# Kernel tuning notes

Measured on AMD Instinct MI355X. Metric: run time of the kernel, lower is better.

## Reference

```python
import jax, jax.numpy as jnp
import numpy as np

L, B, D = 128, 4096, 300


def setup_inputs() -> dict:
    key = jax.random.key(0)
    k1, k2, k3 = jax.random.split(key, 3)
    sentence = jax.random.normal(k1, (L, B, D), dtype=jnp.float32)
    size = jax.random.randint(k2, (B,), 0, L)  # per-example valid lengths
    # nn.Bilinear(D, D, 1, bias=False) weight, squeezed to [D, D]
    W = jax.random.normal(k3, (D, D), dtype=jnp.float32) * (1.0 / np.sqrt(D))
    return {"sentence": sentence, "size": size, "W": W}


def reference(sentence, size, W):
    # sentence: [L, B, D] seq-first; size: [B] lengths; W: [D, D] bilinear weight
    Ls, Bs, Ds = sentence.shape
    dim = jnp.asarray(Ds, sentence.dtype)
    neg_inf = jnp.asarray(-jnp.inf, sentence.dtype)

    def bil(x, y):
        # elementwise bilinear score x^T W y -> [l, b]
        return jnp.einsum('lbd,de,lbe->lb', x, W, y)

    # symmetrized neighbor score for pairs (l, l-1), l = 1..L-1 -> [L-1, B]
    sym = 0.5 * (bil(sentence[1:], sentence[:-1]) + bil(sentence[:-1], sentence[1:]))

    pad = jnp.full((1, Bs), neg_inf, dtype=sentence.dtype)
    w0 = jnp.concatenate([pad, sym], axis=0)   # prev-neighbor channel; l=0 has no prev
    w2 = jnp.concatenate([sym, pad], axis=0)   # next-neighbor channel; l=L-1 has no next
    w1 = bil(sentence, sentence)               # self channel, always valid

    # padding masks from 'size': channel 0 valid for l < size, channel 2 for l < size-1
    pos = jnp.arange(Ls)[:, None]              # [L, 1]
    w0 = jnp.where(pos < size[None, :], w0, neg_inf)
    w2 = jnp.where(pos < jnp.clip(size - 1, 0)[None, :], w2, neg_inf)

    logits = jnp.stack([w0, w1, w2], axis=-1) / dim   # [L, B, 3]
    w = jax.nn.softmax(logits, axis=-1)               # self channel always finite -> safe

    zero_row = jnp.zeros((1, Bs, Ds), sentence.dtype)
    s_prev = jnp.concatenate([zero_row, sentence[:-1]], axis=0)
    s_next = jnp.concatenate([sentence[1:], zero_row], axis=0)

    # masked channels have exactly zero weight, so padded shifts contribute nothing
    out = w[..., 1:2] * sentence + w[..., 0:1] * s_prev + w[..., 2:3] * s_next
    # dropout(p=0.05) is identity in eval mode
    return out
```

## Files before the change

kernel.cpp:

```cpp
#include <hip/hip_runtime.h>
#include <stdint.h>

#define LL 128
#define BB 4096
#define DD 300
#define DP 320
#define SROW 328

typedef __attribute__((ext_vector_type(8))) short short8;
typedef __attribute__((ext_vector_type(4))) float f32x4;

static constexpr int S16_ELEMS = 129 * SROW;
static constexpr int SMEM_BYTES = S16_ELEMS * 2 + 128 * 5 * 4;

__device__ __forceinline__ unsigned short f2bf(float f) {
    unsigned int u = __builtin_bit_cast(unsigned int, f);
    u = (u + 0x7fffu + ((u >> 16) & 1u)) >> 16;
    return (unsigned short)u;
}
__device__ __forceinline__ float bf2f(unsigned short h) {
    unsigned int u = ((unsigned int)h) << 16;
    return __builtin_bit_cast(float, u);
}

__global__ void prep_w_kernel(const float* __restrict__ W, unsigned short* __restrict__ Wb) {
    int i = blockIdx.x * 256 + threadIdx.x;
    if (i >= DP * DP) return;
    int r = i / DP, c = i % DP;
    float v = 0.0f;
    if (r < DD && c < DD) v = 0.5f * (W[r * DD + c] + W[c * DD + r]);
    Wb[i] = f2bf(v);
}

__global__ __launch_bounds__(512) void fused_kernel(
        const float* __restrict__ sent, const int* __restrict__ sizes,
        const unsigned short* __restrict__ Wb, float* __restrict__ out) {
    extern __shared__ char smem[];
    unsigned short* S16 = (unsigned short*)smem;
    float* q1s = (float*)(smem + S16_ELEMS * 2);
    float* q2s = q1s + 128;
    float* w0s = q2s + 128;
    float* w1s = w0s + 128;
    float* w2s = w1s + 128;

    const int b = blockIdx.x;
    const int t = threadIdx.x;

    for (int idx = t; idx < 128 * 75; idx += 512) {
        int row = idx / 75, c4 = idx % 75;
        const float4 v = ((const float4*)(sent + ((size_t)row * BB + b) * DD))[c4];
        ushort4 h;
        h.x = f2bf(v.x); h.y = f2bf(v.y); h.z = f2bf(v.z); h.w = f2bf(v.w);
        *(ushort4*)&S16[row * SROW + c4 * 4] = h;
    }
    for (int r = t; r < 129; r += 512) {
        #pragma unroll
        for (int c = 300; c < SROW; c += 4) {
            ushort4 z; z.x = 0; z.y = 0; z.z = 0; z.w = 0;
            *(ushort4*)&S16[r * SROW + c] = z;
        }
    }
    for (int c4 = t; c4 < 75; c4 += 512) {
        ushort4 z; z.x = 0; z.y = 0; z.z = 0; z.w = 0;
        *(ushort4*)&S16[128 * SROW + c4 * 4] = z;
    }
    if (t < 256) q1s[t] = 0.0f;
    __syncthreads();

    const int lane = t & 63;
    const int wave = t >> 6;
    const int mw = wave & 3;
    const int nw2 = wave >> 2;
    const int lo = lane & 15;
    const int quad = lane >> 4;

    f32x4 acc[5][4];
    #pragma unroll
    for (int i = 0; i < 5; i++)
        #pragma unroll
        for (int j = 0; j < 4; j++)
            acc[i][j] = (f32x4){0.f, 0.f, 0.f, 0.f};

    #pragma unroll
    for (int kc = 0; kc < 10; kc++) {
        short8 Af[5], Bf[4];
        #pragma unroll
        for (int i = 0; i < 5; i++)
            Af[i] = *(const short8*)&Wb[(16 * (5 * mw + i) + lo) * DP + kc * 32 + quad * 8];
        #pragma unroll
        for (int j = 0; j < 4; j++)
            Bf[j] = *(const short8*)&S16[(16 * (4 * nw2 + j) + lo) * SROW + kc * 32 + quad * 8];
        #pragma unroll
        for (int i = 0; i < 5; i++)
            #pragma unroll
            for (int j = 0; j < 4; j++)
                acc[i][j] = __builtin_amdgcn_mfma_f32_16x16x32_bf16(Af[i], Bf[j], acc[i][j], 0, 0, 0);
    }

    float q1v[4] = {0.f, 0.f, 0.f, 0.f};
    float q2v[4] = {0.f, 0.f, 0.f, 0.f};
    #pragma unroll
    for (int i = 0; i < 5; i++) {
        const int d0 = 16 * (5 * mw + i) + quad * 4;
        #pragma unroll
        for (int j = 0; j < 4; j++) {
            const int l = 16 * (4 * nw2 + j) + lo;
            const ushort4 s1 = *(const ushort4*)&S16[l * SROW + d0];
            const ushort4 s2 = *(const ushort4*)&S16[(l + 1) * SROW + d0];
            const f32x4 a = acc[i][j];
            q1v[j] += a[0] * bf2f(s1.x) + a[1] * bf2f(s1.y) + a[2] * bf2f(s1.z) + a[3] * bf2f(s1.w);
            q2v[j] += a[0] * bf2f(s2.x) + a[1] * bf2f(s2.y) + a[2] * bf2f(s2.z) + a[3] * bf2f(s2.w);
        }
    }
    #pragma unroll
    for (int j = 0; j < 4; j++) {
        float v1 = q1v[j], v2 = q2v[j];
        v1 += __shfl_xor(v1, 16); v1 += __shfl_xor(v1, 32);
        v2 += __shfl_xor(v2, 16); v2 += __shfl_xor(v2, 32);
        if (quad == 0) {
            const int l = 16 * (4 * nw2 + j) + lo;
            atomicAdd(&q1s[l], v1);
            atomicAdd(&q2s[l], v2);
        }
    }
    __syncthreads();

    const int sz = sizes[b];
    if (t < 128) {
        const int l = t;
        const float inv_d = 1.0f / 300.0f;
        const float NEG_INF = -__builtin_inff();
        const float a1 = q1s[l] * inv_d;
        const float a0 = (l >= 1 && l < sz) ? q2s[l - 1] * inv_d : NEG_INF;
        const float a2 = (l < LL - 1 && l < sz - 1) ? q2s[l] * inv_d : NEG_INF;
        const float mx = fmaxf(a1, fmaxf(a0, a2));
        const float e0 = __expf(a0 - mx);
        const float e1 = __expf(a1 - mx);
        const float e2 = __expf(a2 - mx);
        const float inv = 1.0f / (e0 + e1 + e2);
        w0s[l] = e0 * inv;
        w1s[l] = e1 * inv;
        w2s[l] = e2 * inv;
    }
    __syncthreads();

    for (int idx = t; idx < 128 * 75; idx += 512) {
        const int l = idx / 75;
        const int d = (idx % 75) * 4;
        const float W0 = w0s[l], W1 = w1s[l], W2 = w2s[l];
        const int lp = (l == 0) ? 0 : l - 1;
        const ushort4 sp = *(const ushort4*)&S16[lp * SROW + d];
        const ushort4 sc = *(const ushort4*)&S16[l * SROW + d];
        const ushort4 sn = *(const ushort4*)&S16[(l + 1) * SROW + d];
        float4 o;
        o.x = W1 * bf2f(sc.x) + W0 * bf2f(sp.x) + W2 * bf2f(sn.x);
        o.y = W1 * bf2f(sc.y) + W0 * bf2f(sp.y) + W2 * bf2f(sn.y);
        o.z = W1 * bf2f(sc.z) + W0 * bf2f(sp.z) + W2 * bf2f(sn.z);
        o.w = W1 * bf2f(sc.w) + W0 * bf2f(sp.w) + W2 * bf2f(sn.w);
        *(float4*)&out[((size_t)l * BB + b) * DD + d] = o;
    }
}

extern "C" void kernel_launch(void* const* d_in, const int* in_sizes, int n_in,
                              void* d_out, int out_size, void* d_ws, size_t ws_size,
                              hipStream_t stream) {
    const float* sent = (const float*)d_in[0];
    const int* sizes  = (const int*)d_in[1];
    const float* W    = (const float*)d_in[2];
    float* out        = (float*)d_out;
    unsigned short* Wb = (unsigned short*)d_ws;

    prep_w_kernel<<<(DP * DP + 255) / 256, 256, 0, stream>>>(W, Wb);

    hipFuncSetAttribute(reinterpret_cast<const void*>(fused_kernel),
                        hipFuncAttributeMaxDynamicSharedMemorySize, SMEM_BYTES);
    fused_kernel<<<BB, 512, SMEM_BYTES, stream>>>(sent, sizes, Wb, out);
}
```

Before: 1.308 ms.

## Split each batch column across two blocks with halo rows to raise occupancy

Each block now handles 64 sequence positions of one batch column instead of all 128, loading 66 rows (one halo row on each side) into shared memory and launching twice as many blocks. This halves LDS use per block and cuts the per-wave accumulator set from 5x4 to 5x2. Together with a launch-bounds occupancy hint, the aim is more resident blocks per CU to hide global-memory latency. The cost is extra halo loads, an extra dot product for the boundary neighbour score, and double the W-fragment reads from global/L2 per batch column.

```diff
diff --git a/kernel.cpp b/kernel.cpp
--- a/kernel.cpp
+++ b/kernel.cpp
@@ -6,12 +6,14 @@
 #define DD 300
 #define DP 320
 #define SROW 328
+#define OWN 64
+#define ROWS 66
 
 typedef __attribute__((ext_vector_type(8))) short short8;
 typedef __attribute__((ext_vector_type(4))) float f32x4;
 
-static constexpr int S16_ELEMS = 129 * SROW;
-static constexpr int SMEM_BYTES = S16_ELEMS * 2 + 128 * 5 * 4;
+static constexpr int S16_ELEMS = ROWS * SROW;
+static constexpr int SMEM_BYTES = S16_ELEMS * 2 + (64 + 65 + 64 + 64 + 64) * 4;
 
 __device__ __forceinline__ unsigned short f2bf(float f) {
     unsigned int u = __builtin_bit_cast(unsigned int, f);
@@ -32,39 +34,38 @@
     Wb[i] = f2bf(v);
 }
 
-__global__ __launch_bounds__(512) void fused_kernel(
+__global__ __launch_bounds__(512, 6) void fused_kernel(
         const float* __restrict__ sent, const int* __restrict__ sizes,
         const unsigned short* __restrict__ Wb, float* __restrict__ out) {
     extern __shared__ char smem[];
     unsigned short* S16 = (unsigned short*)smem;
     float* q1s = (float*)(smem + S16_ELEMS * 2);
-    float* q2s = q1s + 128;
-    float* w0s = q2s + 128;
-    float* w1s = w0s + 128;
-    float* w2s = w1s + 128;
+    float* q2s = q1s + 64;
+    float* w0s = q2s + 65;
+    float* w1s = w0s + 64;
+    float* w2s = w1s + 64;
 
-    const int b = blockIdx.x;
+    const int bid = blockIdx.x;
+    const int b = bid >> 1;
+    const int base = (bid & 1) * OWN;
     const int t = threadIdx.x;
 
-    for (int idx = t; idx < 128 * 75; idx += 512) {
-        int row = idx / 75, c4 = idx % 75;
-        const float4 v = ((const float4*)(sent + ((size_t)row * BB + b) * DD))[c4];
-        ushort4 h;
-        h.x = f2bf(v.x); h.y = f2bf(v.y); h.z = f2bf(v.z); h.w = f2bf(v.w);
-        *(ushort4*)&S16[row * SROW + c4 * 4] = h;
+    for (int idx = t; idx < ROWS * 75; idx += 512) {
+        const int r = idx / 75, c4 = idx % 75;
+        const int g = base - 1 + r;
+        ushort4 h; h.x = 0; h.y = 0; h.z = 0; h.w = 0;
+        if (g >= 0 && g < LL) {
+            const float4 v = ((const float4*)(sent + ((size_t)g * BB + b) * DD))[c4];
+            h.x = f2bf(v.x); h.y = f2bf(v.y); h.z = f2bf(v.z); h.w = f2bf(v.w);
+        }
+        *(ushort4*)&S16[r * SROW + c4 * 4] = h;
     }
-    for (int r = t; r < 129; r += 512) {
-        #pragma unroll
-        for (int c = 300; c < SROW; c += 4) {
-            ushort4 z; z.x = 0; z.y = 0; z.z = 0; z.w = 0;
-            *(ushort4*)&S16[r * SROW + c] = z;
-        }
+    for (int idx = t; idx < ROWS * 7; idx += 512) {
+        const int r = idx / 7, c = 300 + (idx % 7) * 4;
+        ushort4 z; z.x = 0; z.y = 0; z.z = 0; z.w = 0;
+        *(ushort4*)&S16[r * SROW + c] = z;
     }
-    for (int c4 = t; c4 < 75; c4 += 512) {
-        ushort4 z; z.x = 0; z.y = 0; z.z = 0; z.w = 0;
-        *(ushort4*)&S16[128 * SROW + c4 * 4] = z;
-    }
-    if (t < 256) q1s[t] = 0.0f;
+    if (t < 129) q1s[t] = 0.0f;
     __syncthreads();
 
     const int lane = t & 63;
@@ -74,90 +75,94 @@
     const int lo = lane & 15;
     const int quad = lane >> 4;
 
-    f32x4 acc[5][4];
+    f32x4 acc[5][2];
     #pragma unroll
     for (int i = 0; i < 5; i++)
         #pragma unroll
-        for (int j = 0; j < 4; j++)
+        for (int j = 0; j < 2; j++)
             acc[i][j] = (f32x4){0.f, 0.f, 0.f, 0.f};
 
     #pragma unroll
     for (int kc = 0; kc < 10; kc++) {
-        short8 Af[5], Bf[4];
+        short8 Bf[2];
         #pragma unroll
-        for (int i = 0; i < 5; i++)
-            Af[i] = *(const short8*)&Wb[(16 * (5 * mw + i) + lo) * DP + kc * 32 + quad * 8];
+        for (int j = 0; j < 2; j++)
+            Bf[j] = *(const short8*)&S16[(1 + 16 * (2 * nw2 + j) + lo) * SROW + kc * 32 + quad * 8];
         #pragma unroll
-        for (int j = 0; j < 4; j++)
-            Bf[j] = *(const short8*)&S16[(16 * (4 * nw2 + j) + lo) * SROW + kc * 32 + quad * 8];
-        #pragma unroll
-        for (int i = 0; i < 5; i++)
+        for (int i = 0; i < 5; i++) {
+            const short8 Af = *(const short8*)&Wb[(16 * (5 * mw + i) + lo) * DP + kc * 32 + quad * 8];
             #pragma unroll
-            for (int j = 0; j < 4; j++)
-                acc[i][j] = __builtin_amdgcn_mfma_f32_16x16x32_bf16(Af[i], Bf[j], acc[i][j], 0, 0, 0);
+            for (int j = 0; j < 2; j++)
+                acc[i][j] = __builtin_amdgcn_mfma_f32_16x16x32_bf16(Af, Bf[j], acc[i][j], 0, 0, 0);
+        }
     }
 
-    float q1v[4] = {0.f, 0.f, 0.f, 0.f};
-    float q2v[4] = {0.f, 0.f, 0.f, 0.f};
+    float q1v[2] = {0.f, 0.f};
+    float q2v[2] = {0.f, 0.f};
+    float qm = 0.f;
     #pragma unroll
     for (int i = 0; i < 5; i++) {
         const int d0 = 16 * (5 * mw + i) + quad * 4;
+        const ushort4 s0 = *(const ushort4*)&S16[d0];
+        const f32x4 a0 = acc[i][0];
+        qm += a0[0] * bf2f(s0.x) + a0[1] * bf2f(s0.y) + a0[2] * bf2f(s0.z) + a0[3] * bf2f(s0.w);
         #pragma unroll
-        for (int j = 0; j < 4; j++) {
-            const int l = 16 * (4 * nw2 + j) + lo;
-            const ushort4 s1 = *(const ushort4*)&S16[l * SROW + d0];
-            const ushort4 s2 = *(const ushort4*)&S16[(l + 1) * SROW + d0];
+        for (int j = 0; j < 2; j++) {
+            const int ll = 16 * (2 * nw2 + j) + lo;
+            const ushort4 s1 = *(const ushort4*)&S16[(ll + 1) * SROW + d0];
+            const ushort4 s2 = *(const ushort4*)&S16[(ll + 2) * SROW + d0];
             const f32x4 a = acc[i][j];
             q1v[j] += a[0] * bf2f(s1.x) + a[1] * bf2f(s1.y) + a[2] * bf2f(s1.z) + a[3] * bf2f(s1.w);
             q2v[j] += a[0] * bf2f(s2.x) + a[1] * bf2f(s2.y) + a[2] * bf2f(s2.z) + a[3] * bf2f(s2.w);
         }
     }
     #pragma unroll
-    for (int j = 0; j < 4; j++) {
+    for (int j = 0; j < 2; j++) {
         float v1 = q1v[j], v2 = q2v[j];
         v1 += __shfl_xor(v1, 16); v1 += __shfl_xor(v1, 32);
         v2 += __shfl_xor(v2, 16); v2 += __shfl_xor(v2, 32);
         if (quad == 0) {
-            const int l = 16 * (4 * nw2 + j) + lo;
-            atomicAdd(&q1s[l], v1);
-            atomicAdd(&q2s[l], v2);
+            const int ll = 16 * (2 * nw2 + j) + lo;
+            atomicAdd(&q1s[ll], v1);
+            atomicAdd(&q2s[ll + 1], v2);
         }
     }
+    qm += __shfl_xor(qm, 16); qm += __shfl_xor(qm, 32);
+    if (lane == 0 && nw2 == 0) atomicAdd(&q2s[0], qm);
     __syncthreads();
 
     const int sz = sizes[b];
-    if (t < 128) {
-        const int l = t;
+    if (t < OWN) {
+        const int l = base + t;
         const float inv_d = 1.0f / 300.0f;
         const float NEG_INF = -__builtin_inff();
-        const float a1 = q1s[l] * inv_d;
-        const float a0 = (l >= 1 && l < sz) ? q2s[l - 1] * inv_d : NEG_INF;
-        const float a2 = (l < LL - 1 && l < sz - 1) ? q2s[l] * inv_d : NEG_INF;
+        const float a1 = q1s[t] * inv_d;
+        const float a0 = (l >= 1 && l < sz) ? q2s[t] * inv_d : NEG_INF;
+        const float a2 = (l < LL - 1 && l < sz - 1) ? q2s[t + 1] * inv_d : NEG_INF;
         const float mx = fmaxf(a1, fmaxf(a0, a2));
         const float e0 = __expf(a0 - mx);
         const float e1 = __expf(a1 - mx);
         const float e2 = __expf(a2 - mx);
         const float inv = 1.0f / (e0 + e1 + e2);
-        w0s[l] = e0 * inv;
-        w1s[l] = e1 * inv;
-        w2s[l] = e2 * inv;
+        w0s[t] = e0 * inv;
+        w1s[t] = e1 * inv;
+        w2s[t] = e2 * inv;
     }
     __syncthreads();
 
-    for (int idx = t; idx < 128 * 75; idx += 512) {
-        const int l = idx / 75;
+    for (int idx = t; idx < OWN * 75; idx += 512) {
+        const int ll = idx / 75;
         const int d = (idx % 75) * 4;
-        const float W0 = w0s[l], W1 = w1s[l], W2 = w2s[l];
-        const int lp = (l == 0) ? 0 : l - 1;
-        const ushort4 sp = *(const ushort4*)&S16[lp * SROW + d];
-        const ushort4 sc = *(const ushort4*)&S16[l * SROW + d];
-        const ushort4 sn = *(const ushort4*)&S16[(l + 1) * SROW + d];
+        const float W0 = w0s[ll], W1 = w1s[ll], W2 = w2s[ll];
+        const ushort4 sp = *(const ushort4*)&S16[ll * SROW + d];
+        const ushort4 sc = *(const ushort4*)&S16[(ll + 1) * SROW + d];
+        const ushort4 sn = *(const ushort4*)&S16[(ll + 2) * SROW + d];
         float4 o;
         o.x = W1 * bf2f(sc.x) + W0 * bf2f(sp.x) + W2 * bf2f(sn.x);
         o.y = W1 * bf2f(sc.y) + W0 * bf2f(sp.y) + W2 * bf2f(sn.y);
         o.z = W1 * bf2f(sc.z) + W0 * bf2f(sp.z) + W2 * bf2f(sn.z);
         o.w = W1 * bf2f(sc.w) + W0 * bf2f(sp.w) + W2 * bf2f(sn.w);
-        *(float4*)&out[((size_t)l * BB + b) * DD + d] = o;
+        *(float4*)&out[((size_t)(base + ll) * BB + b) * DD + d] = o;
     }
 }
 
@@ -174,5 +179,5 @@
 
     hipFuncSetAttribute(reinterpret_cast<const void*>(fused_kernel),
                         hipFuncAttributeMaxDynamicSharedMemorySize, SMEM_BYTES);
-    fused_kernel<<<BB, 512, SMEM_BYTES, stream>>>(sent, sizes, Wb, out);
+    fused_kernel<<<BB * 2, 512, SMEM_BYTES, stream>>>(sent, sizes, Wb, out);
 }
```

Measured after the change: 1.362 ms. +4.2%, slower.
